# Optimization experiments

Hardware: AMD Instinct MI355X
Metric: run time of the kernel (lower is better)

## Reference

```python
import jax, jax.numpy as jnp
import numpy as np
import math

B, N, C = 1, 2048, 256
H, CH = 8, 32
PQ, PV = 8, 12
CZ = 32
BQ, BK = 32, 128
NB = N // BQ
PAD = (BK - BQ) // 2
INF = 1e8
EPS = 1e-8

_KIDX = np.arange(NB)[:, None] * BQ + np.arange(BK)[None, :] - PAD
_KVALID = (_KIDX >= 0) & (_KIDX < N)
_KIDX_C = np.clip(_KIDX, 0, N - 1)


def _quat_to_rot(q):
    q = q / jnp.linalg.norm(q, axis=-1, keepdims=True)
    w, x, y, z = q[..., 0], q[..., 1], q[..., 2], q[..., 3]
    return jnp.stack([
        jnp.stack([1 - 2 * (y * y + z * z), 2 * (x * y - w * z), 2 * (x * z + w * y)], -1),
        jnp.stack([2 * (x * y + w * z), 1 - 2 * (x * x + z * z), 2 * (y * z - w * x)], -1),
        jnp.stack([2 * (x * z - w * y), 2 * (y * z + w * x), 1 - 2 * (x * x + y * y)], -1)], -2)


def _to_queries(x):
    # [B, N, ...] -> [B, NB, BQ, ...]
    return x.reshape((B, NB, BQ) + x.shape[2:])


def _to_keys(x):
    # [B, N, ...] -> [B, NB, BK, ...] zero-padded sliding key windows
    g = x[:, _KIDX_C]
    v = jnp.asarray(_KVALID, x.dtype).reshape((1, NB, BK) + (1,) * (x.ndim - 2))
    return g * v


def _ln(x):
    m = x.mean(-1, keepdims=True)
    var = x.var(-1, keepdims=True)
    return (x - m) / jnp.sqrt(var + 1e-5)


def setup_inputs():
    key = jax.random.key(0)
    ks = jax.random.split(key, 16)
    p = 0.02
    return {
        's': jax.random.normal(ks[0], (B, N, C), jnp.float32),
        'cond': jax.random.normal(ks[1], (B, N, C), jnp.float32),
        'z': jax.random.normal(ks[2], (B, NB, BQ, BK, CZ), jnp.float32),
        'trans': jax.random.normal(ks[3], (B, N, 3), jnp.float32),
        'rots': _quat_to_rot(jax.random.normal(ks[4], (B, N, 4), jnp.float32)),
        's_mask': jnp.ones((B, N), jnp.float32),
        'Wq': jax.random.normal(ks[5], (C, H * CH)) * p,
        'Wk': jax.random.normal(ks[6], (C, H * CH)) * p,
        'Wv': jax.random.normal(ks[7], (C, H * CH)) * p,
        'Wqp': jax.random.normal(ks[8], (C, H * PQ * 3)) * p,
        'Wkvp': jax.random.normal(ks[9], (C, H * (PQ + PV) * 3)) * p,
        'Wb': jax.random.normal(ks[10], (CZ, H)) * p,
        'Wdz': jax.random.normal(ks[11], (CZ, CZ // 4)) * p,
        'head_weights': jnp.full((H,), 0.5413),
        'Wout': jax.random.normal(ks[12], (H * (CZ // 4 + CH + PV * 4), C)) * p,
        'Wg': jax.random.normal(ks[13], (C, C)) * p,
        'bg': jnp.zeros((C,)),
        'Wbeta': jax.random.normal(ks[14], (C, C)) * p,
        'bbeta': jnp.zeros((C,)),
        'g_z': jnp.ones((CZ,)),
        'b_z': jnp.zeros((CZ,)),
    }


def reference(s, cond, z, trans, rots, s_mask, Wq, Wk, Wv, Wqp, Wkvp, Wb, Wdz,
              head_weights, Wout, Wg, bg, Wbeta, bbeta, g_z, b_z):
    # AdaLN on s conditioned on cond; LayerNorm on z
    s = _ln(s) * (cond @ Wg + bg) + (cond @ Wbeta + bbeta)
    z = _ln(z) * g_z + b_z

    q_in = _to_queries(s)            # [B,NB,BQ,C]
    k_in = _to_keys(s)               # [B,NB,BK,C]
    q_t = _to_queries(trans)         # [B,NB,BQ,3]
    q_R = _to_queries(rots)          # [B,NB,BQ,3,3]
    k_t = _to_keys(trans)
    k_R = _to_keys(rots)
    # zero-padded key rotations -> identity
    zero = jnp.all(k_R == 0, axis=(-2, -1))[..., None, None]
    k_R = jnp.where(zero, jnp.eye(3, dtype=k_R.dtype), k_R)

    q = (q_in @ Wq).reshape(B, NB, BQ, H, CH)
    k = (k_in @ Wk).reshape(B, NB, BK, H, CH)
    v = (k_in @ Wv).reshape(B, NB, BK, H, CH)

    q_pts = (q_in @ Wqp).reshape(B, NB, BQ, H * PQ, 3)
    q_pts = jnp.einsum('bnqij,bnqpj->bnqpi', q_R, q_pts) + q_t[..., None, :]
    q_pts = q_pts.reshape(B, NB, BQ, H, PQ, 3)

    kv_pts = (k_in @ Wkvp).reshape(B, NB, BK, H * (PQ + PV), 3)
    kv_pts = jnp.einsum('bnkij,bnkpj->bnkpi', k_R, kv_pts) + k_t[..., None, :]
    kv_pts = kv_pts.reshape(B, NB, BK, H, PQ + PV, 3)
    k_pts, v_pts = kv_pts[..., :PQ, :], kv_pts[..., PQ:, :]

    b = z @ Wb                                    # [B,NB,BQ,BK,H]
    a = jnp.einsum('bnqhc,bnkhc->bnqkh', q, k) * math.sqrt(1.0 / (3 * CH))
    a = a + math.sqrt(1.0 / 3.0) * b

    disp = q_pts[:, :, :, None] - k_pts[:, :, None]   # [B,NB,BQ,BK,H,PQ,3]
    d2 = jnp.sum(disp * disp, axis=-1)                # [B,NB,BQ,BK,H,PQ]
    hw = jax.nn.softplus(head_weights) * math.sqrt(1.0 / (3 * (PQ * 9.0 / 2)))
    pt_att = -0.5 * jnp.sum(d2 * hw[:, None], axis=-1)   # [B,NB,BQ,BK,H]

    m_q = _to_queries(s_mask[..., None])              # [B,NB,BQ,1]
    m_k = _to_keys(s_mask[..., None])                 # [B,NB,BK,1]
    attn_mask = m_q * jnp.swapaxes(m_k, -1, -2)       # [B,NB,BQ,BK]
    attn_mask = INF * (attn_mask - 1.0)

    a = a + pt_att + attn_mask[..., None]
    a = jnp.swapaxes(a, -1, -2)                       # [B,NB,BQ,H,BK]
    a = jax.nn.softmax(a, axis=-1)

    o = jnp.einsum('bnqhk,bnkhc->bnqhc', a, v).reshape(B, NB, BQ, H * CH)
    o_pt = jnp.einsum('bnqhk,bnkhvc->bnqhvc', a, v_pts)      # [B,NB,BQ,H,PV,3]
    o_pt = jnp.einsum('bnqji,bnqhvj->bnqhvi', q_R,
                      o_pt - q_t[:, :, :, None, None, :])     # invert apply
    o_pt_norm = jnp.sqrt(jnp.sum(o_pt ** 2, -1) + EPS).reshape(B, NB, BQ, H * PV)
    o_pt = o_pt.reshape(B, NB, BQ, H * PV * 3)
    pair_z = z @ Wdz                                          # [B,NB,BQ,BK,CZ//4]
    o_pair = jnp.einsum('bnqhk,bnqkc->bnqhc', a, pair_z).reshape(B, NB, BQ, H * (CZ // 4))

    out = jnp.concatenate([o, o_pt, o_pt_norm, o_pair], -1) @ Wout
    return out.reshape(B, N, C)
```

## Files before the change

### kernel.cpp

```cpp
#include <hip/hip_runtime.h>
#include <hip/hip_bf16.h>
#include <math.h>

typedef __hip_bfloat16 bf16;
typedef __attribute__((ext_vector_type(8))) short short8;
typedef __attribute__((ext_vector_type(4))) float f32x4;

#define NRES 2048
#define CDIM 256
#define PADK 48
#define POS 1440

static __device__ __forceinline__ float b2f(bf16 x) { return __bfloat162float(x); }
static __device__ __forceinline__ float us2f(short u) {
    return __uint_as_float(((unsigned)(unsigned short)u) << 16);
}
static __device__ __forceinline__ short f2s(float f) {
    bf16 h = __float2bfloat16(f);
    return *reinterpret_cast<short*>(&h);
}
static __device__ __forceinline__ bool flag_f32(const void* smask) {
    return *(const unsigned int*)smask == 0x3F800000u;
}
static __device__ __forceinline__ float dual_load(const void* p, size_t i, bool f32) {
    float vf = ((const float*)p)[f32 ? i : 0];
    float vb = b2f(((const bf16*)p)[f32 ? (size_t)0 : i]);
    return f32 ? vf : vb;
}

struct PrepTable {
    const void* src[8];
    bf16* dst[8];
    int srcN[8];
    int nOff[8];
    int dstStride[8];
    float scl[8];
    int tileOff[9];
    const void* s;
    const void* cond;
    bf16* condb;
    bf16* xnb;
};
__global__ __launch_bounds__(256) void k_prep(PrepTable tb, const void* __restrict__ smask) {
    bool f32 = flag_f32(smask);
    int b = blockIdx.x;
    int t = threadIdx.x;
    if (b < tb.tileOff[8]) {
        int s = 0;
        while (b >= tb.tileOff[s + 1]) ++s;
        int rel = b - tb.tileOff[s];
        int ntTiles = tb.srcN[s] >> 5;
        int kt = rel / ntTiles, nt = rel % ntTiles;
        const void* src = tb.src[s];
        int srcN = tb.srcN[s];
        float scl = tb.scl[s];
        __shared__ float tile[32][33];
        int tx = t & 31, ty = t >> 5;
#pragma unroll
        for (int r = 0; r < 4; ++r) {
            int srow = kt * 32 + ty + r * 8;
            int scol = nt * 32 + tx;
            tile[ty + r * 8][tx] = dual_load(src, (size_t)srow * srcN + scol, f32);
        }
        __syncthreads();
        bf16* dst = tb.dst[s];
#pragma unroll
        for (int r = 0; r < 4; ++r) {
            int n = nt * 32 + ty + r * 8 + tb.nOff[s];
            int k = kt * 32 + tx;
            dst[(size_t)n * tb.dstStride[s] + k] = __float2bfloat16(tile[tx][ty + r * 8] * scl);
        }
        return;
    }
    b -= tb.tileOff[8];
    if (b < 256) {
        int i0 = b * 2048;
        for (int i = t; i < 2048; i += 256)
            tb.condb[i0 + i] = __float2bfloat16(dual_load(tb.cond, (size_t)(i0 + i), f32));
        return;
    }
    b -= 256;
    __shared__ float ls[8][CDIM];
    __shared__ float mrs[8][2];
    int r0 = b * 8;
    for (int i = t; i < 8 * CDIM; i += 256) {
        int r = i >> 8, c = i & 255;
        ls[r][c] = dual_load(tb.s, (size_t)(r0 + r) * CDIM + c, f32);
    }
    __syncthreads();
    int wave = t >> 6, lane = t & 63;
    for (int rr = 0; rr < 2; ++rr) {
        int r = wave * 2 + rr;
        float sum = 0.f, sq = 0.f;
        for (int j = lane; j < CDIM; j += 64) { float v = ls[r][j]; sum += v; sq += v * v; }
        for (int off = 32; off; off >>= 1) { sum += __shfl_xor(sum, off); sq += __shfl_xor(sq, off); }
        if (lane == 0) {
            float m = sum / CDIM;
            float var = fmaxf(sq / CDIM - m * m, 0.f);
            mrs[r][0] = m; mrs[r][1] = rsqrtf(var + 1e-5f);
        }
    }
    __syncthreads();
    int c = t;
#pragma unroll
    for (int r = 0; r < 8; ++r)
        tb.xnb[(size_t)(r0 + r) * CDIM + c] = __float2bfloat16((ls[r][c] - mrs[r][0]) * mrs[r][1]);
}

__global__ __launch_bounds__(256) void k_gb(
    const bf16* __restrict__ condb, const bf16* __restrict__ GWt, const bf16* __restrict__ xnb,
    const void* __restrict__ bg, const void* __restrict__ bbeta,
    const void* __restrict__ smask, bf16* __restrict__ SQb)
{
    bool f32 = flag_f32(smask);
    int wid = threadIdx.x >> 6, lane = threadIdx.x & 63;
    int tid = blockIdx.x * 4 + wid;
    int mt = tid >> 4, nt = tid & 15;
    int idx = lane & 15, quad = lane >> 4;
    const bf16* Ap = condb + (size_t)(mt * 16 + idx) * 256 + quad * 8;
    const bf16* B0 = GWt + (size_t)(nt * 16 + idx) * 256 + quad * 8;
    const bf16* B1 = GWt + (size_t)(256 + nt * 16 + idx) * 256 + quad * 8;
    f32x4 a0 = {0,0,0,0}, a1 = {0,0,0,0};
    for (int k = 0; k < 256; k += 32) {
        short8 af = *(const short8*)(Ap + k);
        a0 = __builtin_amdgcn_mfma_f32_16x16x32_bf16(af, *(const short8*)(B0 + k), a0, 0, 0, 0);
        a1 = __builtin_amdgcn_mfma_f32_16x16x32_bf16(af, *(const short8*)(B1 + k), a1, 0, 0, 0);
    }
    int ocol = nt * 16 + idx;
    float bgc = dual_load(bg, ocol, f32), bbc = dual_load(bbeta, ocol, f32);
    int orow = mt * 16 + quad * 4;
#pragma unroll
    for (int r = 0; r < 4; ++r) {
        int row = orow + r;
        float xn = b2f(xnb[(size_t)row * 256 + ocol]);
        SQb[(size_t)row * 256 + ocol] = __float2bfloat16(xn * (a0[r] + bgc) + (a1[r] + bbc));
    }
}

__global__ __launch_bounds__(256) void k_gemm22b(
    const bf16* __restrict__ A, const bf16* __restrict__ Bt, bf16* __restrict__ C,
    int N, int K, int totalWaves)
{
    int wid = threadIdx.x >> 6, lane = threadIdx.x & 63;
    int tid = blockIdx.x * 4 + wid;
    if (tid >= totalWaves) return;
    int tiles_n = N >> 5;
    int mt = tid / tiles_n, nt = tid % tiles_n;
    int idx = lane & 15, quad = lane >> 4;
    const bf16* Ap0 = A + (size_t)(mt * 32 + idx) * K + quad * 8;
    const bf16* Ap1 = Ap0 + (size_t)16 * K;
    const bf16* Bp0 = Bt + (size_t)(nt * 32 + idx) * K + quad * 8;
    const bf16* Bp1 = Bp0 + (size_t)16 * K;
    f32x4 a00 = {0,0,0,0}, a01 = {0,0,0,0}, a10 = {0,0,0,0}, a11 = {0,0,0,0};
    for (int k = 0; k < K; k += 32) {
        short8 af0 = *(const short8*)(Ap0 + k);
        short8 af1 = *(const short8*)(Ap1 + k);
        short8 bf0 = *(const short8*)(Bp0 + k);
        short8 bf1 = *(const short8*)(Bp1 + k);
        a00 = __builtin_amdgcn_mfma_f32_16x16x32_bf16(af0, bf0, a00, 0, 0, 0);
        a01 = __builtin_amdgcn_mfma_f32_16x16x32_bf16(af0, bf1, a01, 0, 0, 0);
        a10 = __builtin_amdgcn_mfma_f32_16x16x32_bf16(af1, bf0, a10, 0, 0, 0);
        a11 = __builtin_amdgcn_mfma_f32_16x16x32_bf16(af1, bf1, a11, 0, 0, 0);
    }
    int orow = mt * 32 + quad * 4;
    int ocol = nt * 32 + idx;
#pragma unroll
    for (int r = 0; r < 4; ++r) {
        C[(size_t)(orow + r) * N + ocol] = __float2bfloat16(a00[r]);
        C[(size_t)(orow + r) * N + ocol + 16] = __float2bfloat16(a01[r]);
        C[(size_t)(orow + r + 16) * N + ocol] = __float2bfloat16(a10[r]);
        C[(size_t)(orow + r + 16) * N + ocol + 16] = __float2bfloat16(a11[r]);
    }
}

__global__ __launch_bounds__(256) void k_z(
    const void* __restrict__ z, const void* __restrict__ Wb, const void* __restrict__ Wdz,
    const void* __restrict__ g_z, const void* __restrict__ b_z,
    const void* __restrict__ smask,
    bf16* __restrict__ Bzb, bf16* __restrict__ PZb)
{
    __shared__ float wb[32][8], wdz[32][8], gz[32], bz[32];
    bool f32 = flag_f32(smask);
    int t = threadIdx.x;
    {
        int j = t >> 3, c = t & 7;
        wb[j][c] = 0.5773502691896258f * dual_load(Wb, t, f32);
        wdz[j][c] = dual_load(Wdz, t, f32);
    }
    if (t < 32) { gz[t] = dual_load(g_z, t, f32); bz[t] = dual_load(b_z, t, f32); }
    __syncthreads();
    size_t r = (size_t)blockIdx.x * 256 + t;
    float zv[32];
    float sum = 0.f, sq = 0.f;
    if (f32) {
        const float4* zp = (const float4*)((const float*)z + r * 32);
#pragma unroll
        for (int j4 = 0; j4 < 8; ++j4) {
            float4 v4 = zp[j4];
            zv[j4 * 4 + 0] = v4.x; zv[j4 * 4 + 1] = v4.y; zv[j4 * 4 + 2] = v4.z; zv[j4 * 4 + 3] = v4.w;
        }
    } else {
        const bf16* zp = (const bf16*)z + r * 32;
#pragma unroll
        for (int j = 0; j < 32; ++j) zv[j] = b2f(zp[j]);
    }
#pragma unroll
    for (int j = 0; j < 32; ++j) { float v = zv[j]; sum += v; sq += v * v; }
    float m = sum / 32.f;
    float var = fmaxf(sq / 32.f - m * m, 0.f);
    float rstd = rsqrtf(var + 1e-5f);
#pragma unroll
    for (int j = 0; j < 32; ++j) zv[j] = (zv[j] - m) * rstd * gz[j] + bz[j];
    float bacc[8], pacc[8];
#pragma unroll
    for (int c = 0; c < 8; ++c) { bacc[c] = 0.f; pacc[c] = 0.f; }
    for (int j = 0; j < 32; ++j) {
        float v = zv[j];
#pragma unroll
        for (int c = 0; c < 8; ++c) { bacc[c] += v * wb[j][c]; pacc[c] += v * wdz[j][c]; }
    }
    int n = (int)(r >> 12);
    int q = (int)(r >> 7) & 31;
    int k = (int)r & 127;
#pragma unroll
    for (int h = 0; h < 8; ++h)
        Bzb[(size_t)n * 32768 + (size_t)h * 4096 + q * 128 + k] = __float2bfloat16(bacc[h]);
#pragma unroll
    for (int c = 0; c < 8; ++c)
        PZb[(((size_t)(n * 32 + q)) * 8 + c) * 128 + k] = __float2bfloat16(pacc[c]);
}

__global__ __launch_bounds__(256) void k_attn_out(
    const bf16* __restrict__ POb,
    const bf16* __restrict__ Bzb, const bf16* __restrict__ PZb,
    const void* __restrict__ rots, const void* __restrict__ trans,
    const void* __restrict__ smask, const void* __restrict__ head_weights,
    bf16* __restrict__ CATb)
{
    __shared__ char buf[70016];
    __shared__ float rowq[32], rowk[128], mk[128], mqv[32];
    short* QfS = (short*)buf;
    short* KfS = (short*)(buf + 4608);
    short* VtS = (short*)(buf + 23040);
    short* AsS = (short*)(buf + 44800);
    float* S   = (float*)(buf + 53504);
    float* OPT = (float*)(buf + 53504);

    const int n = blockIdx.x >> 3, h = blockIdx.x & 7;
    const int t = threadIdx.x;
    const bool f32 = flag_f32(smask);
    const int n32 = n * 32;

    float hwv = dual_load(head_weights, h, f32);
    float ptc = -0.5f * log1pf(expf(hwv)) * 0.09622504486493764f;
    float m2ptc = -2.f * ptc;
    const short8 zero8 = {0,0,0,0,0,0,0,0};

    if (t < 128) {
        int q = t >> 2, g = t & 3;
        *(short8*)(QfS + q * 72 + g * 8) =
            *(const short8*)(POb + (size_t)(n32 + q) * POS + h * 32 + g * 8);
    }
    for (int i = t; i < 512; i += 256) {
        int k = i >> 2, g = i & 3;
        int kg = n32 + k - PADK;
        short8 v = zero8;
        if (kg >= 0 && kg < NRES)
            v = *(const short8*)(POb + (size_t)kg * POS + 256 + h * 32 + g * 8);
        *(short8*)(KfS + k * 72 + g * 8) = v;
    }
    for (int i = t; i < 512; i += 256) {
        int k = i >> 2, g = i & 3;
        int kg = n32 + k - PADK;
        short8 v = zero8;
        if (kg >= 0 && kg < NRES)
            v = *(const short8*)(POb + (size_t)kg * POS + 512 + h * 32 + g * 8);
#pragma unroll
        for (int j = 0; j < 8; ++j) VtS[(g * 8 + j) * 136 + k] = v[j];
    }
    for (int i = t; i < 320; i += 256) {
        if (i < 64) { int q = i >> 1, g = i & 1; *(short8*)(QfS + q * 72 + 56 + g * 8) = zero8; }
        else { int j = i - 64; int k = j >> 1, g = j & 1; *(short8*)(KfS + k * 72 + 56 + g * 8) = zero8; }
    }
    for (int i = t; i < 204; i += 256) {
        int r = 68 + i / 17, sg = i % 17;
        *(short8*)(VtS + r * 136 + sg * 8) = zero8;
    }
    if (t >= 64 && t < 192) {
        int k = t - 64;
        int kg = n32 + k - PADK;
        bool valid = (kg >= 0 && kg < NRES);
        float mv = 0.f, s2 = 0.f;
        if (valid) {
            float R[9], T[3];
#pragma unroll
            for (int d = 0; d < 9; ++d) R[d] = dual_load(rots, (size_t)kg * 9 + d, f32);
#pragma unroll
            for (int d = 0; d < 3; ++d) T[d] = dual_load(trans, (size_t)kg * 3 + d, f32);
            mv = dual_load(smask, kg, f32);
            const bf16* kv = POb + (size_t)kg * POS + 960 + h * 60;
#pragma unroll
            for (int j = 0; j < 20; ++j) {
                float x = b2f(kv[j * 3]), y = b2f(kv[j * 3 + 1]), z = b2f(kv[j * 3 + 2]);
                float p0 = R[0] * x + R[1] * y + R[2] * z + T[0];
                float p1 = R[3] * x + R[4] * y + R[5] * z + T[1];
                float p2 = R[6] * x + R[7] * y + R[8] * z + T[2];
                if (j < 8) {
                    KfS[k * 72 + 32 + j * 3 + 0] = f2s(p0);
                    KfS[k * 72 + 32 + j * 3 + 1] = f2s(p1);
                    KfS[k * 72 + 32 + j * 3 + 2] = f2s(p2);
                    s2 += p0 * p0 + p1 * p1 + p2 * p2;
                } else {
                    int v = j - 8;
                    VtS[(32 + v * 3 + 0) * 136 + k] = f2s(p0);
                    VtS[(32 + v * 3 + 1) * 136 + k] = f2s(p1);
                    VtS[(32 + v * 3 + 2) * 136 + k] = f2s(p2);
                }
            }
        } else {
            for (int c = 32; c < 56; ++c) KfS[k * 72 + c] = 0;
            for (int x = 32; x < 68; ++x) VtS[x * 136 + k] = 0;
        }
        rowk[k] = ptc * s2;
        mk[k] = mv;
    } else if (t >= 224) {
        int q = t - 224;
        int g = n32 + q;
        float R[9], T[3];
#pragma unroll
        for (int d = 0; d < 9; ++d) R[d] = dual_load(rots, (size_t)g * 9 + d, f32);
#pragma unroll
        for (int d = 0; d < 3; ++d) T[d] = dual_load(trans, (size_t)g * 3 + d, f32);
        mqv[q] = dual_load(smask, g, f32);
        const bf16* qv = POb + (size_t)g * POS + 768 + h * 24;
        float s2 = 0.f;
#pragma unroll
        for (int p = 0; p < 8; ++p) {
            float x = b2f(qv[p * 3]), y = b2f(qv[p * 3 + 1]), z = b2f(qv[p * 3 + 2]);
            float p0 = R[0] * x + R[1] * y + R[2] * z + T[0];
            float p1 = R[3] * x + R[4] * y + R[5] * z + T[1];
            float p2 = R[6] * x + R[7] * y + R[8] * z + T[2];
            QfS[q * 72 + 32 + p * 3 + 0] = f2s(m2ptc * p0);
            QfS[q * 72 + 32 + p * 3 + 1] = f2s(m2ptc * p1);
            QfS[q * 72 + 32 + p * 3 + 2] = f2s(m2ptc * p2);
            s2 += p0 * p0 + p1 * p1 + p2 * p2;
        }
        rowq[q] = ptc * s2;
    }
    __syncthreads();

    const int wid = t >> 6, lane = t & 63, idx = lane & 15, quad = lane >> 4;
#pragma unroll
    for (int i = 0; i < 4; ++i) {
        int tt = wid * 4 + i;
        int mt = tt >> 3, nt = tt & 7;
        f32x4 acc = {0.f, 0.f, 0.f, 0.f};
#pragma unroll
        for (int kk = 0; kk < 2; ++kk) {
            short8 af  = *(const short8*)(QfS + (mt * 16 + idx) * 72 + kk * 32 + quad * 8);
            short8 bfv = *(const short8*)(KfS + (nt * 16 + idx) * 72 + kk * 32 + quad * 8);
            acc = __builtin_amdgcn_mfma_f32_16x16x32_bf16(af, bfv, acc, 0, 0, 0);
        }
#pragma unroll
        for (int r = 0; r < 4; ++r) {
            int q = mt * 16 + quad * 4 + r;
            int k = nt * 16 + idx;
            float bz = b2f(Bzb[(size_t)n * 32768 + (size_t)h * 4096 + q * 128 + k]);
            float msk = 1e8f * (mqv[q] * mk[k] - 1.f);
            S[q * 129 + k] = acc[r] + bz + rowq[q] + rowk[k] + msk;
        }
    }
    __syncthreads();

    for (int rr = 0; rr < 8; ++rr) {
        int q = wid * 8 + rr;
        float v0 = S[q * 129 + lane], v1 = S[q * 129 + lane + 64];
        float mx = fmaxf(v0, v1);
        for (int off = 32; off; off >>= 1) mx = fmaxf(mx, __shfl_xor(mx, off));
        float e0 = expf(v0 - mx), e1 = expf(v1 - mx);
        float sm = e0 + e1;
        for (int off = 32; off; off >>= 1) sm += __shfl_xor(sm, off);
        float inv = 1.f / sm;
        AsS[q * 136 + lane] = f2s(e0 * inv);
        AsS[q * 136 + lane + 64] = f2s(e1 * inv);
    }
    __syncthreads();

    {
        int q = t >> 3, c = t & 7;
        const short8* pzp = (const short8*)(PZb + ((size_t)(n32 + q) * 8 + c) * 128);
        const short8* asp = (const short8*)(AsS + q * 136);
        float acc = 0.f;
        for (int k8 = 0; k8 < 16; ++k8) {
            short8 pv = pzp[k8];
            short8 av = asp[k8];
#pragma unroll
            for (int j = 0; j < 8; ++j) acc += us2f(av[j]) * us2f(pv[j]);
        }
        CATb[(size_t)(n32 + q) * 704 + 640 + h * 8 + c] = __float2bfloat16(acc);
    }
#pragma unroll
    for (int i = 0; i < 3; ++i) {
        int tt = wid + i * 4;
        if (tt >= 10) break;
        int mt = tt / 5, nt = tt % 5;
        f32x4 acc = {0.f, 0.f, 0.f, 0.f};
#pragma unroll
        for (int kk = 0; kk < 4; ++kk) {
            short8 af  = *(const short8*)(AsS + (mt * 16 + idx) * 136 + kk * 32 + quad * 8);
            short8 bfv = *(const short8*)(VtS + (nt * 16 + idx) * 136 + kk * 32 + quad * 8);
            acc = __builtin_amdgcn_mfma_f32_16x16x32_bf16(af, bfv, acc, 0, 0, 0);
        }
        int x = nt * 16 + idx;
#pragma unroll
        for (int r = 0; r < 4; ++r) {
            int q = mt * 16 + quad * 4 + r;
            if (x < 32)
                CATb[(size_t)(n32 + q) * 704 + h * 32 + x] = __float2bfloat16(acc[r]);
            else if (x < 68)
                OPT[q * 37 + (x - 32)] = acc[r];
        }
    }
    __syncthreads();

    for (int i = t; i < 32 * 12; i += 256) {
        int q = i / 12, v = i % 12;
        int g = n32 + q;
        float R[9], T[3];
#pragma unroll
        for (int d = 0; d < 9; ++d) R[d] = dual_load(rots, (size_t)g * 9 + d, f32);
#pragma unroll
        for (int d = 0; d < 3; ++d) T[d] = dual_load(trans, (size_t)g * 3 + d, f32);
        float x = OPT[q * 37 + v * 3 + 0] - T[0];
        float y = OPT[q * 37 + v * 3 + 1] - T[1];
        float z = OPT[q * 37 + v * 3 + 2] - T[2];
        float o0 = R[0] * x + R[3] * y + R[6] * z;
        float o1 = R[1] * x + R[4] * y + R[7] * z;
        float o2 = R[2] * x + R[5] * y + R[8] * z;
        size_t cb = (size_t)g * 704;
        CATb[cb + 256 + (h * 12 + v) * 3 + 0] = __float2bfloat16(o0);
        CATb[cb + 256 + (h * 12 + v) * 3 + 1] = __float2bfloat16(o1);
        CATb[cb + 256 + (h * 12 + v) * 3 + 2] = __float2bfloat16(o2);
        CATb[cb + 544 + h * 12 + v] = __float2bfloat16(sqrtf(o0 * o0 + o1 * o1 + o2 * o2 + 1e-8f));
    }
}

__global__ __launch_bounds__(256) void k_gemm(
    const bf16* __restrict__ A, const bf16* __restrict__ Bt, void* __restrict__ Cv,
    int N, int K, int totalTiles, const void* __restrict__ smask)
{
    int wid = threadIdx.x >> 6, lane = threadIdx.x & 63;
    int tid = blockIdx.x * 4 + wid;
    if (tid >= totalTiles) return;
    int tiles_n = N >> 4;
    int mt = tid / tiles_n, nt = tid % tiles_n;
    int idx = lane & 15, quad = lane >> 4;
    const bf16* Ap = A + (size_t)(mt * 16 + idx) * K + quad * 8;
    const bf16* Bp = Bt + (size_t)(nt * 16 + idx) * K + quad * 8;
    f32x4 acc = {0.f, 0.f, 0.f, 0.f};
    for (int k = 0; k < K; k += 32) {
        short8 af = *(const short8*)(Ap + k);
        short8 bfv = *(const short8*)(Bp + k);
        acc = __builtin_amdgcn_mfma_f32_16x16x32_bf16(af, bfv, acc, 0, 0, 0);
    }
    int orow = mt * 16 + quad * 4;
    int ocol = nt * 16 + idx;
    if (flag_f32(smask)) {
        float* C = (float*)Cv;
#pragma unroll
        for (int r = 0; r < 4; ++r) C[(size_t)(orow + r) * N + ocol] = acc[r];
    } else {
        bf16* C = (bf16*)Cv;
#pragma unroll
        for (int r = 0; r < 4; ++r) C[(size_t)(orow + r) * N + ocol] = __float2bfloat16(acc[r]);
    }
}

extern "C" void kernel_launch(void* const* d_in, const int* in_sizes, int n_in,
                              void* d_out, int out_size, void* d_ws, size_t ws_size,
                              hipStream_t stream) {
    const void* s       = d_in[0];
    const void* cond    = d_in[1];
    const void* z       = d_in[2];
    const void* trans   = d_in[3];
    const void* rots    = d_in[4];
    const void* s_mask  = d_in[5];
    const void* Wq      = d_in[6];
    const void* Wk      = d_in[7];
    const void* Wv      = d_in[8];
    const void* Wqp     = d_in[9];
    const void* Wkvp    = d_in[10];
    const void* Wb      = d_in[11];
    const void* Wdz     = d_in[12];
    const void* hweights= d_in[13];
    const void* Wout    = d_in[14];
    const void* Wg      = d_in[15];
    const void* bg      = d_in[16];
    const void* Wbeta   = d_in[17];
    const void* bbeta   = d_in[18];
    const void* g_z     = d_in[19];
    const void* b_z     = d_in[20];

    float* ws = (float*)d_ws;
    bf16* POb   = (bf16*)(ws);
    bf16* Bzb   = (bf16*)(ws + 1474560);
    bf16* PZb   = (bf16*)(ws + 2523136);
    bf16* SQb   = (bf16*)(ws + 3571712);
    bf16* condb = (bf16*)(ws + 3833856);
    bf16* xnb   = (bf16*)(ws + 4096000);
    bf16* CATb  = (bf16*)(ws + 4358144);
    bf16* PWt   = (bf16*)(ws + 5079040);
    bf16* GWt   = (bf16*)(ws + 5263360);
    bf16* FWt   = (bf16*)(ws + 5328896);

    PrepTable tb;
    const float qkscale = 0.10206207261596575f;
    tb.src[0] = Wq;   tb.dst[0] = PWt; tb.srcN[0] = 256; tb.nOff[0] = 0;   tb.dstStride[0] = 256; tb.scl[0] = qkscale;
    tb.src[1] = Wk;   tb.dst[1] = PWt; tb.srcN[1] = 256; tb.nOff[1] = 256; tb.dstStride[1] = 256; tb.scl[1] = 1.f;
    tb.src[2] = Wv;   tb.dst[2] = PWt; tb.srcN[2] = 256; tb.nOff[2] = 512; tb.dstStride[2] = 256; tb.scl[2] = 1.f;
    tb.src[3] = Wqp;  tb.dst[3] = PWt; tb.srcN[3] = 192; tb.nOff[3] = 768; tb.dstStride[3] = 256; tb.scl[3] = 1.f;
    tb.src[4] = Wkvp; tb.dst[4] = PWt; tb.srcN[4] = 480; tb.nOff[4] = 960; tb.dstStride[4] = 256; tb.scl[4] = 1.f;
    tb.src[5] = Wg;   tb.dst[5] = GWt; tb.srcN[5] = 256; tb.nOff[5] = 0;   tb.dstStride[5] = 256; tb.scl[5] = 1.f;
    tb.src[6] = Wbeta;tb.dst[6] = GWt; tb.srcN[6] = 256; tb.nOff[6] = 256; tb.dstStride[6] = 256; tb.scl[6] = 1.f;
    tb.src[7] = Wout; tb.dst[7] = FWt; tb.srcN[7] = 256; tb.nOff[7] = 0;   tb.dstStride[7] = 704; tb.scl[7] = 1.f;
    int tc[8] = {64, 64, 64, 48, 120, 64, 64, 176};
    tb.tileOff[0] = 0;
    for (int i = 0; i < 8; ++i) tb.tileOff[i + 1] = tb.tileOff[i] + tc[i];
    tb.s = s; tb.cond = cond; tb.condb = condb; tb.xnb = xnb;

    dim3 blk(256);
    k_prep<<<dim3(664 + 256 + 256), blk, 0, stream>>>(tb, s_mask);
    k_gb<<<dim3(512), blk, 0, stream>>>(condb, GWt, xnb, bg, bbeta, s_mask, SQb);
    k_gemm22b<<<dim3(720), blk, 0, stream>>>(SQb, PWt, POb, 1440, 256, 2880);
    k_z<<<dim3(1024), blk, 0, stream>>>(z, Wb, Wdz, g_z, b_z, s_mask, Bzb, PZb);
    k_attn_out<<<dim3(512), blk, 0, stream>>>(POb, Bzb, PZb, rots, trans, s_mask, hweights, CATb);
    k_gemm<<<dim3(512), blk, 0, stream>>>(CATb, FWt, d_out, 256, 704, 2048, s_mask);
}
```

Baseline: 177.4 us.

## Fuse pair-feature kernel into prep and stage rigid frames and points in shared memory

The separate z-processing kernel (layernorm of the pair tensor plus the bias and Wdz projections) now runs as extra blocks of the prep kernel. This removes one launch and lets that work overlap the weight transposes and the input layernorm. The prep kernel also packs rotations and translations into a 12-float per-residue table, so the attention kernel can read a frame with three float4 loads instead of twelve scalar dual-format loads. The attention kernel now stages key and query point coordinates in shared memory with vector loads and splits the per-key point transform across two threads. The cost is a larger prep grid, more shared memory in the prep kernel, and an extra __syncthreads in the attention kernel.

```diff
diff --git a/kernel.cpp b/kernel.cpp
--- a/kernel.cpp
+++ b/kernel.cpp
@@ -4,6 +4,7 @@
 
 typedef __hip_bfloat16 bf16;
 typedef __attribute__((ext_vector_type(8))) short short8;
+typedef __attribute__((ext_vector_type(4))) short short4v;
 typedef __attribute__((ext_vector_type(4))) float f32x4;
 
 #define NRES 2048
@@ -40,8 +41,22 @@
     const void* cond;
     bf16* condb;
     bf16* xnb;
+    const void* rots;
+    const void* trans;
+    float* RT;
+    const void* z;
+    const void* Wb;
+    const void* Wdz;
+    const void* g_z;
+    const void* b_z;
+    bf16* Bzb;
+    bf16* PZb;
 };
 __global__ __launch_bounds__(256) void k_prep(PrepTable tb, const void* __restrict__ smask) {
+    __shared__ float tile[32][33];
+    __shared__ float ls[8][CDIM];
+    __shared__ float mrs[8][2];
+    __shared__ float wb[32][8], wdz[32][8], gz[32], bz[32];
     bool f32 = flag_f32(smask);
     int b = blockIdx.x;
     int t = threadIdx.x;
@@ -54,7 +69,6 @@
         const void* src = tb.src[s];
         int srcN = tb.srcN[s];
         float scl = tb.scl[s];
-        __shared__ float tile[32][33];
         int tx = t & 31, ty = t >> 5;
 #pragma unroll
         for (int r = 0; r < 4; ++r) {
@@ -80,31 +94,88 @@
         return;
     }
     b -= 256;
-    __shared__ float ls[8][CDIM];
-    __shared__ float mrs[8][2];
-    int r0 = b * 8;
-    for (int i = t; i < 8 * CDIM; i += 256) {
-        int r = i >> 8, c = i & 255;
-        ls[r][c] = dual_load(tb.s, (size_t)(r0 + r) * CDIM + c, f32);
-    }
+    if (b < 256) {
+        int r0 = b * 8;
+        for (int i = t; i < 8 * CDIM; i += 256) {
+            int r = i >> 8, c = i & 255;
+            ls[r][c] = dual_load(tb.s, (size_t)(r0 + r) * CDIM + c, f32);
+        }
+        __syncthreads();
+        int wave = t >> 6, lane = t & 63;
+        for (int rr = 0; rr < 2; ++rr) {
+            int r = wave * 2 + rr;
+            float sum = 0.f, sq = 0.f;
+            for (int j = lane; j < CDIM; j += 64) { float v = ls[r][j]; sum += v; sq += v * v; }
+            for (int off = 32; off; off >>= 1) { sum += __shfl_xor(sum, off); sq += __shfl_xor(sq, off); }
+            if (lane == 0) {
+                float m = sum / CDIM;
+                float var = fmaxf(sq / CDIM - m * m, 0.f);
+                mrs[r][0] = m; mrs[r][1] = rsqrtf(var + 1e-5f);
+            }
+        }
+        __syncthreads();
+        int c = t;
+#pragma unroll
+        for (int r = 0; r < 8; ++r)
+            tb.xnb[(size_t)(r0 + r) * CDIM + c] = __float2bfloat16((ls[r][c] - mrs[r][0]) * mrs[r][1]);
+        return;
+    }
+    b -= 256;
+    if (b < 96) {
+        int i = b * 256 + t;
+        int row = i / 12, c = i % 12;
+        float v = (c < 9) ? dual_load(tb.rots, (size_t)row * 9 + c, f32)
+                          : dual_load(tb.trans, (size_t)row * 3 + (c - 9), f32);
+        tb.RT[i] = v;
+        return;
+    }
+    b -= 96;
+    {
+        int j = t >> 3, c = t & 7;
+        wb[j][c] = 0.5773502691896258f * dual_load(tb.Wb, t, f32);
+        wdz[j][c] = dual_load(tb.Wdz, t, f32);
+    }
+    if (t < 32) { gz[t] = dual_load(tb.g_z, t, f32); bz[t] = dual_load(tb.b_z, t, f32); }
     __syncthreads();
-    int wave = t >> 6, lane = t & 63;
-    for (int rr = 0; rr < 2; ++rr) {
-        int r = wave * 2 + rr;
-        float sum = 0.f, sq = 0.f;
-        for (int j = lane; j < CDIM; j += 64) { float v = ls[r][j]; sum += v; sq += v * v; }
-        for (int off = 32; off; off >>= 1) { sum += __shfl_xor(sum, off); sq += __shfl_xor(sq, off); }
-        if (lane == 0) {
-            float m = sum / CDIM;
-            float var = fmaxf(sq / CDIM - m * m, 0.f);
-            mrs[r][0] = m; mrs[r][1] = rsqrtf(var + 1e-5f);
-        }
-    }
-    __syncthreads();
-    int c = t;
-#pragma unroll
-    for (int r = 0; r < 8; ++r)
-        tb.xnb[(size_t)(r0 + r) * CDIM + c] = __float2bfloat16((ls[r][c] - mrs[r][0]) * mrs[r][1]);
+    size_t r = (size_t)b * 256 + t;
+    float zv[32];
+    float sum = 0.f, sq = 0.f;
+    if (f32) {
+        const float4* zp = (const float4*)((const float*)tb.z + r * 32);
+#pragma unroll
+        for (int j4 = 0; j4 < 8; ++j4) {
+            float4 v4 = zp[j4];
+            zv[j4 * 4 + 0] = v4.x; zv[j4 * 4 + 1] = v4.y; zv[j4 * 4 + 2] = v4.z; zv[j4 * 4 + 3] = v4.w;
+        }
+    } else {
+        const bf16* zp = (const bf16*)tb.z + r * 32;
+#pragma unroll
+        for (int j = 0; j < 32; ++j) zv[j] = b2f(zp[j]);
+    }
+#pragma unroll
+    for (int j = 0; j < 32; ++j) { float v = zv[j]; sum += v; sq += v * v; }
+    float m = sum / 32.f;
+    float var = fmaxf(sq / 32.f - m * m, 0.f);
+    float rstd = rsqrtf(var + 1e-5f);
+#pragma unroll
+    for (int j = 0; j < 32; ++j) zv[j] = (zv[j] - m) * rstd * gz[j] + bz[j];
+    float bacc[8], pacc[8];
+#pragma unroll
+    for (int c = 0; c < 8; ++c) { bacc[c] = 0.f; pacc[c] = 0.f; }
+    for (int j = 0; j < 32; ++j) {
+        float v = zv[j];
+#pragma unroll
+        for (int c = 0; c < 8; ++c) { bacc[c] += v * wb[j][c]; pacc[c] += v * wdz[j][c]; }
+    }
+    int n = (int)(r >> 12);
+    int q = (int)(r >> 7) & 31;
+    int k = (int)r & 127;
+#pragma unroll
+    for (int h = 0; h < 8; ++h)
+        tb.Bzb[(size_t)n * 32768 + (size_t)h * 4096 + q * 128 + k] = __float2bfloat16(bacc[h]);
+#pragma unroll
+    for (int c = 0; c < 8; ++c)
+        tb.PZb[(((size_t)(n * 32 + q)) * 8 + c) * 128 + k] = __float2bfloat16(pacc[c]);
 }
 
 __global__ __launch_bounds__(256) void k_gb(
@@ -173,67 +244,10 @@
     }
 }
 
-__global__ __launch_bounds__(256) void k_z(
-    const void* __restrict__ z, const void* __restrict__ Wb, const void* __restrict__ Wdz,
-    const void* __restrict__ g_z, const void* __restrict__ b_z,
-    const void* __restrict__ smask,
-    bf16* __restrict__ Bzb, bf16* __restrict__ PZb)
-{
-    __shared__ float wb[32][8], wdz[32][8], gz[32], bz[32];
-    bool f32 = flag_f32(smask);
-    int t = threadIdx.x;
-    {
-        int j = t >> 3, c = t & 7;
-        wb[j][c] = 0.5773502691896258f * dual_load(Wb, t, f32);
-        wdz[j][c] = dual_load(Wdz, t, f32);
-    }
-    if (t < 32) { gz[t] = dual_load(g_z, t, f32); bz[t] = dual_load(b_z, t, f32); }
-    __syncthreads();
-    size_t r = (size_t)blockIdx.x * 256 + t;
-    float zv[32];
-    float sum = 0.f, sq = 0.f;
-    if (f32) {
-        const float4* zp = (const float4*)((const float*)z + r * 32);
-#pragma unroll
-        for (int j4 = 0; j4 < 8; ++j4) {
-            float4 v4 = zp[j4];
-            zv[j4 * 4 + 0] = v4.x; zv[j4 * 4 + 1] = v4.y; zv[j4 * 4 + 2] = v4.z; zv[j4 * 4 + 3] = v4.w;
-        }
-    } else {
-        const bf16* zp = (const bf16*)z + r * 32;
-#pragma unroll
-        for (int j = 0; j < 32; ++j) zv[j] = b2f(zp[j]);
-    }
-#pragma unroll
-    for (int j = 0; j < 32; ++j) { float v = zv[j]; sum += v; sq += v * v; }
-    float m = sum / 32.f;
-    float var = fmaxf(sq / 32.f - m * m, 0.f);
-    float rstd = rsqrtf(var + 1e-5f);
-#pragma unroll
-    for (int j = 0; j < 32; ++j) zv[j] = (zv[j] - m) * rstd * gz[j] + bz[j];
-    float bacc[8], pacc[8];
-#pragma unroll
-    for (int c = 0; c < 8; ++c) { bacc[c] = 0.f; pacc[c] = 0.f; }
-    for (int j = 0; j < 32; ++j) {
-        float v = zv[j];
-#pragma unroll
-        for (int c = 0; c < 8; ++c) { bacc[c] += v * wb[j][c]; pacc[c] += v * wdz[j][c]; }
-    }
-    int n = (int)(r >> 12);
-    int q = (int)(r >> 7) & 31;
-    int k = (int)r & 127;
-#pragma unroll
-    for (int h = 0; h < 8; ++h)
-        Bzb[(size_t)n * 32768 + (size_t)h * 4096 + q * 128 + k] = __float2bfloat16(bacc[h]);
-#pragma unroll
-    for (int c = 0; c < 8; ++c)
-        PZb[(((size_t)(n * 32 + q)) * 8 + c) * 128 + k] = __float2bfloat16(pacc[c]);
-}
-
 __global__ __launch_bounds__(256) void k_attn_out(
     const bf16* __restrict__ POb,
     const bf16* __restrict__ Bzb, const bf16* __restrict__ PZb,
-    const void* __restrict__ rots, const void* __restrict__ trans,
+    const float* __restrict__ RT,
     const void* __restrict__ smask, const void* __restrict__ head_weights,
     bf16* __restrict__ CATb)
 {
@@ -245,6 +259,8 @@
     short* AsS = (short*)(buf + 44800);
     float* S   = (float*)(buf + 53504);
     float* OPT = (float*)(buf + 53504);
+    short* PtsS = (short*)(buf + 44800);
+    short* QpS  = (short*)(buf + 62208);
 
     const int n = blockIdx.x >> 3, h = blockIdx.x & 7;
     const int t = threadIdx.x;
@@ -255,6 +271,7 @@
     float ptc = -0.5f * log1pf(expf(hwv)) * 0.09622504486493764f;
     float m2ptc = -2.f * ptc;
     const short8 zero8 = {0,0,0,0,0,0,0,0};
+    const short4v zero4 = {0,0,0,0};
 
     if (t < 128) {
         int q = t >> 2, g = t & 3;
@@ -278,6 +295,19 @@
 #pragma unroll
         for (int j = 0; j < 8; ++j) VtS[(g * 8 + j) * 136 + k] = v[j];
     }
+    for (int i = t; i < 1920; i += 256) {
+        int k = i / 15, g = i % 15;
+        int kg = n32 + k - PADK;
+        short4v v = zero4;
+        if (kg >= 0 && kg < NRES)
+            v = *(const short4v*)(POb + (size_t)kg * POS + 960 + h * 60 + g * 4);
+        *(short4v*)(PtsS + k * 68 + g * 4) = v;
+    }
+    if (t < 192) {
+        int q = t / 6, g = t % 6;
+        *(short4v*)(QpS + q * 28 + g * 4) =
+            *(const short4v*)(POb + (size_t)(n32 + q) * POS + 768 + h * 24 + g * 4);
+    }
     for (int i = t; i < 320; i += 256) {
         if (i < 64) { int q = i >> 1, g = i & 1; *(short8*)(QfS + q * 72 + 56 + g * 8) = zero8; }
         else { int j = i - 64; int k = j >> 1, g = j & 1; *(short8*)(KfS + k * 72 + 56 + g * 8) = zero8; }
@@ -286,25 +316,26 @@
         int r = 68 + i / 17, sg = i % 17;
         *(short8*)(VtS + r * 136 + sg * 8) = zero8;
     }
-    if (t >= 64 && t < 192) {
-        int k = t - 64;
+    __syncthreads();
+
+    {
+        int k = t >> 1, half = t & 1;
         int kg = n32 + k - PADK;
         bool valid = (kg >= 0 && kg < NRES);
-        float mv = 0.f, s2 = 0.f;
         if (valid) {
-            float R[9], T[3];
-#pragma unroll
-            for (int d = 0; d < 9; ++d) R[d] = dual_load(rots, (size_t)kg * 9 + d, f32);
-#pragma unroll
-            for (int d = 0; d < 3; ++d) T[d] = dual_load(trans, (size_t)kg * 3 + d, f32);
-            mv = dual_load(smask, kg, f32);
-            const bf16* kv = POb + (size_t)kg * POS + 960 + h * 60;
-#pragma unroll
-            for (int j = 0; j < 20; ++j) {
-                float x = b2f(kv[j * 3]), y = b2f(kv[j * 3 + 1]), z = b2f(kv[j * 3 + 2]);
-                float p0 = R[0] * x + R[1] * y + R[2] * z + T[0];
-                float p1 = R[3] * x + R[4] * y + R[5] * z + T[1];
-                float p2 = R[6] * x + R[7] * y + R[8] * z + T[2];
+            const float4* rt = (const float4*)(RT + (size_t)kg * 12);
+            float4 r0 = rt[0], r1 = rt[1], r2 = rt[2];
+            float s2 = 0.f;
+            int j0 = half * 10;
+#pragma unroll
+            for (int jj = 0; jj < 10; ++jj) {
+                int j = j0 + jj;
+                float x = us2f(PtsS[k * 68 + j * 3 + 0]);
+                float y = us2f(PtsS[k * 68 + j * 3 + 1]);
+                float z = us2f(PtsS[k * 68 + j * 3 + 2]);
+                float p0 = r0.x * x + r0.y * y + r0.z * z + r2.y;
+                float p1 = r0.w * x + r1.x * y + r1.y * z + r2.z;
+                float p2 = r1.z * x + r1.w * y + r2.x * z + r2.w;
                 if (j < 8) {
                     KfS[k * 72 + 32 + j * 3 + 0] = f2s(p0);
                     KfS[k * 72 + 32 + j * 3 + 1] = f2s(p1);
@@ -317,29 +348,35 @@
                     VtS[(32 + v * 3 + 2) * 136 + k] = f2s(p2);
                 }
             }
+            if (half == 0) {
+                rowk[k] = ptc * s2;
+                mk[k] = dual_load(smask, kg, f32);
+            }
         } else {
-            for (int c = 32; c < 56; ++c) KfS[k * 72 + c] = 0;
-            for (int x = 32; x < 68; ++x) VtS[x * 136 + k] = 0;
-        }
-        rowk[k] = ptc * s2;
-        mk[k] = mv;
-    } else if (t >= 224) {
-        int q = t - 224;
+            if (half == 0) {
+                for (int c = 32; c < 56; ++c) KfS[k * 72 + c] = 0;
+                for (int x = 32; x < 50; ++x) VtS[x * 136 + k] = 0;
+                rowk[k] = 0.f; mk[k] = 0.f;
+            } else {
+                for (int x = 50; x < 68; ++x) VtS[x * 136 + k] = 0;
+            }
+        }
+    }
+    if (t < 32) {
+        int q = t;
         int g = n32 + q;
-        float R[9], T[3];
-#pragma unroll
-        for (int d = 0; d < 9; ++d) R[d] = dual_load(rots, (size_t)g * 9 + d, f32);
-#pragma unroll
-        for (int d = 0; d < 3; ++d) T[d] = dual_load(trans, (size_t)g * 3 + d, f32);
+        const float4* rt = (const float4*)(RT + (size_t)g * 12);
+        float4 r0 = rt[0], r1 = rt[1], r2 = rt[2];
         mqv[q] = dual_load(smask, g, f32);
-        const bf16* qv = POb + (size_t)g * POS + 768 + h * 24;
         float s2 = 0.f;
 #pragma unroll
         for (int p = 0; p < 8; ++p) {
-            float x = b2f(qv[p * 3]), y = b2f(qv[p * 3 + 1]), z = b2f(qv[p * 3 + 2]);
-            float p0 = R[0] * x + R[1] * y + R[2] * z + T[0];
-            float p1 = R[3] * x + R[4] * y + R[5] * z + T[1];
-            float p2 = R[6] * x + R[7] * y + R[8] * z + T[2];
+            float x = us2f(QpS[q * 28 + p * 3 + 0]);
+            float y = us2f(QpS[q * 28 + p * 3 + 1]);
+            float z = us2f(QpS[q * 28 + p * 3 + 2]);
+            float p0 = r0.x * x + r0.y * y + r0.z * z + r2.y;
+            float p1 = r0.w * x + r1.x * y + r1.y * z + r2.z;
+            float p2 = r1.z * x + r1.w * y + r2.x * z + r2.w;
             QfS[q * 72 + 32 + p * 3 + 0] = f2s(m2ptc * p0);
             QfS[q * 72 + 32 + p * 3 + 1] = f2s(m2ptc * p1);
             QfS[q * 72 + 32 + p * 3 + 2] = f2s(m2ptc * p2);
@@ -423,20 +460,17 @@
     }
     __syncthreads();
 
-    for (int i = t; i < 32 * 12; i += 256) {
+    for (int i = t; i < 384; i += 256) {
         int q = i / 12, v = i % 12;
         int g = n32 + q;
-        float R[9], T[3];
-#pragma unroll
-        for (int d = 0; d < 9; ++d) R[d] = dual_load(rots, (size_t)g * 9 + d, f32);
-#pragma unroll
-        for (int d = 0; d < 3; ++d) T[d] = dual_load(trans, (size_t)g * 3 + d, f32);
-        float x = OPT[q * 37 + v * 3 + 0] - T[0];
-        float y = OPT[q * 37 + v * 3 + 1] - T[1];
-        float z = OPT[q * 37 + v * 3 + 2] - T[2];
-        float o0 = R[0] * x + R[3] * y + R[6] * z;
-        float o1 = R[1] * x + R[4] * y + R[7] * z;
-        float o2 = R[2] * x + R[5] * y + R[8] * z;
+        const float4* rt = (const float4*)(RT + (size_t)g * 12);
+        float4 r0 = rt[0], r1 = rt[1], r2 = rt[2];
+        float x = OPT[q * 37 + v * 3 + 0] - r2.y;
+        float y = OPT[q * 37 + v * 3 + 1] - r2.z;
+        float z = OPT[q * 37 + v * 3 + 2] - r2.w;
+        float o0 = r0.x * x + r0.w * y + r1.z * z;
+        float o1 = r0.y * x + r1.x * y + r1.w * z;
+        float o2 = r0.z * x + r1.y * y + r2.x * z;
         size_t cb = (size_t)g * 704;
         CATb[cb + 256 + (h * 12 + v) * 3 + 0] = __float2bfloat16(o0);
         CATb[cb + 256 + (h * 12 + v) * 3 + 1] = __float2bfloat16(o1);
@@ -512,6 +546,7 @@
     bf16* PWt   = (bf16*)(ws + 5079040);
     bf16* GWt   = (bf16*)(ws + 5263360);
     bf16* FWt   = (bf16*)(ws + 5328896);
+    float* RT   = (float*)(ws + 5419008);
 
     PrepTable tb;
     const float qkscale = 0.10206207261596575f;
@@ -527,12 +562,14 @@
     tb.tileOff[0] = 0;
     for (int i = 0; i < 8; ++i) tb.tileOff[i + 1] = tb.tileOff[i] + tc[i];
     tb.s = s; tb.cond = cond; tb.condb = condb; tb.xnb = xnb;
+    tb.rots = rots; tb.trans = trans; tb.RT = RT;
+    tb.z = z; tb.Wb = Wb; tb.Wdz = Wdz; tb.g_z = g_z; tb.b_z = b_z;
+    tb.Bzb = Bzb; tb.PZb = PZb;
 
     dim3 blk(256);
-    k_prep<<<dim3(664 + 256 + 256), blk, 0, stream>>>(tb, s_mask);
+    k_prep<<<dim3(2296), blk, 0, stream>>>(tb, s_mask);
     k_gb<<<dim3(512), blk, 0, stream>>>(condb, GWt, xnb, bg, bbeta, s_mask, SQb);
     k_gemm22b<<<dim3(720), blk, 0, stream>>>(SQb, PWt, POb, 1440, 256, 2880);
-    k_z<<<dim3(1024), blk, 0, stream>>>(z, Wb, Wdz, g_z, b_z, s_mask, Bzb, PZb);
-    k_attn_out<<<dim3(512), blk, 0, stream>>>(POb, Bzb, PZb, rots, trans, s_mask, hweights, CATb);
+    k_attn_out<<<dim3(512), blk, 0, stream>>>(POb, Bzb, PZb, RT, s_mask, hweights, CATb);
     k_gemm<<<dim3(512), blk, 0, stream>>>(CATb, FWt, d_out, 256, 704, 2048, s_mask);
 }
```

Measured after the change: 177.5 us. Within noise of the previous version (+0.1%).
